# Kernel optimization log

Hardware: AMD Instinct MI355X
Metric: run time of the kernel (lower is better)

## Reference

```python
import jax, jax.numpy as jnp
import numpy as np
import math

V, S, E, H, L, B = 50257, 1024, 768, 12, 12, 4
D = E // H
EPS = 1e-5


def setup_inputs() -> dict:
    key = jax.random.key(0)
    ks = jax.random.split(key, 20)
    sd = 0.02
    inp = {
        "idx": jax.random.randint(ks[0], (B, S), 0, V),
        "targets": jax.random.randint(ks[1], (B, S), 0, V),
        "wte": jax.random.normal(ks[2], (V, E), jnp.float32) * sd,  # tied with lm_head
        "wpe": jax.random.normal(ks[3], (S, E), jnp.float32) * sd,
        "ln1_g": jnp.ones((L, E), jnp.float32),
        "ln1_b": jnp.zeros((L, E), jnp.float32),
        "attn_w": jax.random.normal(ks[4], (L, E, 3 * E), jnp.float32) * sd,
        "attn_b": jnp.zeros((L, 3 * E), jnp.float32),
        "proj_w": jax.random.normal(ks[5], (L, E, E), jnp.float32) * (sd / math.sqrt(2 * L)),
        "proj_b": jnp.zeros((L, E), jnp.float32),
        "ln2_g": jnp.ones((L, E), jnp.float32),
        "ln2_b": jnp.zeros((L, E), jnp.float32),
        "fc_w": jax.random.normal(ks[6], (L, E, 4 * E), jnp.float32) * sd,
        "fc_b": jnp.zeros((L, 4 * E), jnp.float32),
        "fcp_w": jax.random.normal(ks[7], (L, 4 * E, E), jnp.float32) * (sd / math.sqrt(2 * L)),
        "fcp_b": jnp.zeros((L, E), jnp.float32),
        "lnf_g": jnp.ones((E,), jnp.float32),
        "lnf_b": jnp.zeros((E,), jnp.float32),
    }
    return inp


def layer_norm(x, g, b):
    mu = jnp.mean(x, axis=-1, keepdims=True)
    var = jnp.mean(jnp.square(x - mu), axis=-1, keepdims=True)
    return (x - mu) * jax.lax.rsqrt(var + EPS) * g + b


def reference(idx, targets, wte, wpe, ln1_g, ln1_b, attn_w, attn_b, proj_w, proj_b,
              ln2_g, ln2_b, fc_w, fc_b, fcp_w, fcp_b, lnf_g, lnf_b):
    seq = idx.shape[1]
    x = wte[idx] + wpe[:seq]  # [B,S,E]
    mask = jnp.tril(jnp.ones((seq, seq), bool))
    scale = 1.0 / math.sqrt(D)

    def block(x, p):
        l1g, l1b, aw, ab, pw, pb, l2g, l2b, fw, fb, fpw, fpb = p
        h = layer_norm(x, l1g, l1b)
        qkv = h @ aw + ab  # [B,S,3E]
        q, k, v = jnp.split(qkv, 3, axis=-1)
        q = q.reshape(-1, seq, H, D).transpose(0, 2, 1, 3)  # [B,H,S,D]
        k = k.reshape(-1, seq, H, D).transpose(0, 2, 1, 3)
        v = v.reshape(-1, seq, H, D).transpose(0, 2, 1, 3)
        scores = jnp.einsum('bhqd,bhkd->bhqk', q, k) * scale
        scores = jnp.where(mask, scores, -jnp.inf)
        attn = jax.nn.softmax(scores, axis=-1)
        y = jnp.einsum('bhqk,bhkd->bhqd', attn, v)
        y = y.transpose(0, 2, 1, 3).reshape(-1, seq, E)
        x = x + y @ pw + pb
        h2 = layer_norm(x, l2g, l2b)
        h2 = jax.nn.gelu(h2 @ fw + fb, approximate=False)
        x = x + h2 @ fpw + fpb
        return x, None

    x, _ = jax.lax.scan(block, x, (ln1_g, ln1_b, attn_w, attn_b, proj_w, proj_b,
                                   ln2_g, ln2_b, fc_w, fc_b, fcp_w, fcp_b))
    x = layer_norm(x, lnf_g, lnf_b)
    logits = x @ wte.T  # tied lm_head, [B,S,V]
    logp = jax.nn.log_softmax(logits, axis=-1)
    loss = -jnp.mean(jnp.take_along_axis(logp, targets[..., None], axis=-1))
    return logits, loss
```

## Files before the change

### kernel.cpp

```cpp
#include <hip/hip_runtime.h>
#include <hip/hip_bf16.h>
#include <math.h>

#define V 50257
#define SQ 1024
#define E 768
#define NH 12
#define NL 12
#define NB 4
#define MR (NB*SQ)

typedef __bf16 bf16x8 __attribute__((ext_vector_type(8)));
typedef float f32x4 __attribute__((ext_vector_type(4)));
typedef unsigned short us8 __attribute__((ext_vector_type(8)));

__device__ __forceinline__ float b2f(unsigned short u) {
    union { float f; unsigned int i; } x; x.i = ((unsigned int)u) << 16; return x.f;
}
__device__ __forceinline__ unsigned short f2b(float f) {
    unsigned int u = __float_as_uint(f);
    u = (u + 0x7fff + ((u >> 16) & 1)) >> 16;
    return (unsigned short)u;
}
__device__ __forceinline__ void gload16(const unsigned short* g, unsigned short* l) {
    __builtin_amdgcn_global_load_lds((const __attribute__((address_space(1))) void*)g,
                                     (__attribute__((address_space(3))) void*)l, 16, 0, 0);
}

__global__ __launch_bounds__(256)
void embed_k(const int* __restrict__ idx, const float* __restrict__ wte,
             const float* __restrict__ wpe, float* __restrict__ x)
{
    int r = blockIdx.x, t = threadIdx.x;
    int tok = idx[r];
    int s = r & (SQ - 1);
    const float* wt = wte + (size_t)tok * E;
    const float* wp = wpe + (size_t)s * E;
    float* xr = x + (size_t)r * E;
    for (int e = t; e < E; e += 256) xr[e] = wt[e] + wp[e];
}

__global__ __launch_bounds__(256)
void ln_k(const float* __restrict__ x, const float* __restrict__ g,
          const float* __restrict__ bb, unsigned short* __restrict__ out)
{
    int r = blockIdx.x, t = threadIdx.x;
    int lane = t & 63, wid = t >> 6;
    const float* xr = x + (size_t)r * E;
    float v0 = xr[t], v1 = xr[t + 256], v2 = xr[t + 512];
    float s = v0 + v1 + v2;
    #pragma unroll
    for (int o = 1; o < 64; o <<= 1) s += __shfl_xor(s, o);
    __shared__ float red[8];
    if (lane == 0) red[wid] = s;
    __syncthreads();
    float mu = (red[0] + red[1] + red[2] + red[3]) * (1.f / E);
    float d0 = v0 - mu, d1 = v1 - mu, d2 = v2 - mu;
    float s2 = d0 * d0 + d1 * d1 + d2 * d2;
    #pragma unroll
    for (int o = 1; o < 64; o <<= 1) s2 += __shfl_xor(s2, o);
    if (lane == 0) red[wid + 4] = s2;
    __syncthreads();
    float rs = rsqrtf((red[4] + red[5] + red[6] + red[7]) * (1.f / E) + 1e-5f);
    unsigned short* orow = out + (size_t)r * E;
    orow[t]       = f2b(d0 * rs * g[t] + bb[t]);
    orow[t + 256] = f2b(d1 * rs * g[t + 256] + bb[t + 256]);
    orow[t + 512] = f2b(d2 * rs * g[t + 512] + bb[t + 512]);
}

__global__ __launch_bounds__(256)
void conv_k(const float* __restrict__ in, unsigned short* __restrict__ out, int n4)
{
    int i = blockIdx.x * 256 + threadIdx.x;
    int stride = gridDim.x * 256;
    for (; i < n4; i += stride) {
        float4 v = ((const float4*)in)[i];
        ushort4 o;
        o.x = f2b(v.x); o.y = f2b(v.y); o.z = f2b(v.z); o.w = f2b(v.w);
        ((ushort4*)out)[i] = o;
    }
}

__global__ __launch_bounds__(256)
void tconv_k(const float* __restrict__ in, unsigned short* __restrict__ out, int Kd, int Nd)
{
    __shared__ float tile[32][33];
    size_t loff = (size_t)blockIdx.z * Kd * Nd;
    in  += loff;
    out += loff;
    int n0 = blockIdx.x * 32, k0 = blockIdx.y * 32;
    int tc = threadIdx.x & 31, tr = threadIdx.x >> 5;
    #pragma unroll
    for (int i = 0; i < 4; ++i)
        tile[tr + i * 8][tc] = in[(size_t)(k0 + tr + i * 8) * Nd + n0 + tc];
    __syncthreads();
    #pragma unroll
    for (int i = 0; i < 4; ++i)
        out[(size_t)(n0 + tr + i * 8) * Kd + k0 + tc] = f2b(tile[tc][tr + i * 8]);
}

template<int EPI, bool DB, int MI, int NI, int MINW>
__global__ __launch_bounds__(256, MINW)
void gemm_k(const unsigned short* __restrict__ A, const unsigned short* __restrict__ B,
            const float* __restrict__ bias, const float* __restrict__ resid,
            void* __restrict__ Cv, unsigned short* __restrict__ vt,
            float2* __restrict__ part, int M, int N, int K, int Nreal)
{
    constexpr int NBUF = DB ? 2 : 1;
    constexpr int BM = 32 * MI, BN = 32 * NI;
    __shared__ __align__(16) unsigned short As[NBUF][BM * 64];
    __shared__ __align__(16) unsigned short Bs[NBUF][BN * 64];
    const int t = threadIdx.x;
    const int lane = t & 63, wv = t >> 6;
    const int wr = wv >> 1, wc = wv & 1;
    const int m0 = blockIdx.x * BM, n0 = blockIdx.y * BN;
    const int ntile = blockIdx.y;
    const int lq = lane & 15, lg = lane >> 4;

    f32x4 acc[MI][NI];
    const f32x4 fz = {0.f, 0.f, 0.f, 0.f};
    #pragma unroll
    for (int i = 0; i < MI; ++i)
        #pragma unroll
        for (int j = 0; j < NI; ++j) acc[i][j] = fz;

    const int srow = t >> 3, sc = t & 7;

    auto stage = [&](int buf, int k0) {
        #pragma unroll
        for (int i = 0; i < MI; ++i) {
            int row = srow + i * 32;
            int gc = ((sc ^ (row & 7)) << 3);
            gload16(A + (size_t)(m0 + row) * K + k0 + gc, &As[buf][row * 64 + sc * 8]);
        }
        #pragma unroll
        for (int i = 0; i < NI; ++i) {
            int row = srow + i * 32;
            int gc = ((sc ^ (row & 7)) << 3);
            int nrow = n0 + row;
            if (EPI == 3 && nrow >= Nreal) nrow = Nreal - 1;
            gload16(B + (size_t)nrow * K + k0 + gc, &Bs[buf][row * 64 + sc * 8]);
        }
    };
    auto compute = [&](int buf) {
        #pragma unroll
        for (int ks = 0; ks < 64; ks += 32) {
            bf16x8 af[MI], bfr[NI];
            #pragma unroll
            for (int mi = 0; mi < MI; ++mi) {
                int row = wr * (16 * MI) + mi * 16 + lq;
                int c = (ks >> 3) + lg;
                af[mi] = *(const bf16x8*)&As[buf][row * 64 + ((c ^ (row & 7)) << 3)];
            }
            #pragma unroll
            for (int ni = 0; ni < NI; ++ni) {
                int row = wc * (16 * NI) + ni * 16 + lq;
                int c = (ks >> 3) + lg;
                bfr[ni] = *(const bf16x8*)&Bs[buf][row * 64 + ((c ^ (row & 7)) << 3)];
            }
            #pragma unroll
            for (int mi = 0; mi < MI; ++mi)
                #pragma unroll
                for (int ni = 0; ni < NI; ++ni)
                    acc[mi][ni] = __builtin_amdgcn_mfma_f32_16x16x32_bf16(
                        af[mi], bfr[ni], acc[mi][ni], 0, 0, 0);
        }
    };

    const int KT = K >> 6;
    if constexpr (DB) {
        stage(0, 0);
        __syncthreads();
        int cur = 0;
        for (int kt = 0; kt < KT; ++kt) {
            if (kt + 1 < KT) stage(cur ^ 1, (kt + 1) << 6);
            compute(cur);
            __syncthreads();
            cur ^= 1;
        }
    } else {
        for (int kt = 0; kt < KT; ++kt) {
            stage(0, kt << 6);
            __syncthreads();
            compute(0);
            __syncthreads();
        }
    }

    const int colb = n0 + wc * (16 * NI) + lq;
    const int rowb = m0 + wr * (16 * MI) + lg * 4;

    if constexpr (EPI == 3) {
        __shared__ float2 Ls[2][BM / 2][2];
        float* C = (float*)Cv;
        #pragma unroll
        for (int mi = 0; mi < MI; ++mi) {
            #pragma unroll
            for (int j = 0; j < 4; ++j) {
                int row = rowb + mi * 16 + j;
                float v[NI];
                #pragma unroll
                for (int ni = 0; ni < NI; ++ni) {
                    int col = colb + ni * 16;
                    float vv = acc[mi][ni][j];
                    if (col < Nreal) C[(size_t)row * Nreal + col] = vv;
                    else vv = -1e30f;
                    v[ni] = vv;
                }
                float lm = v[0];
                #pragma unroll
                for (int ni = 1; ni < NI; ++ni) lm = fmaxf(lm, v[ni]);
                #pragma unroll
                for (int o = 1; o < 16; o <<= 1) lm = fmaxf(lm, __shfl_xor(lm, o));
                float ls = 0.f;
                #pragma unroll
                for (int ni = 0; ni < NI; ++ni) ls += __expf(v[ni] - lm);
                #pragma unroll
                for (int o = 1; o < 16; o <<= 1) ls += __shfl_xor(ls, o);
                if (lq == 0) Ls[wr][mi * 16 + lg * 4 + j][wc] = make_float2(lm, ls);
            }
        }
        __syncthreads();
        if (t < BM) {
            float2 a = Ls[t / (BM / 2)][t % (BM / 2)][0];
            float2 b = Ls[t / (BM / 2)][t % (BM / 2)][1];
            float mm = fmaxf(a.x, b.x);
            float ss = a.y * __expf(a.x - mm) + b.y * __expf(b.x - mm);
            part[(size_t)ntile * MR + m0 + t] = make_float2(mm, ss);
        }
    } else if constexpr (EPI == 0) {
        unsigned short* C = (unsigned short*)Cv;
        #pragma unroll
        for (int mi = 0; mi < MI; ++mi) {
            int r0 = rowb + mi * 16;
            #pragma unroll
            for (int ni = 0; ni < NI; ++ni) {
                int col = colb + ni * 16;
                float b4 = bias[col];
                float vals[4];
                #pragma unroll
                for (int j = 0; j < 4; ++j) vals[j] = acc[mi][ni][j] + b4;
                #pragma unroll
                for (int j = 0; j < 4; ++j)
                    C[(size_t)(r0 + j) * N + col] = f2b(vals[j]);
                if (col >= 2 * E) {
                    int d = col - 2 * E; int hh = d >> 6; d &= 63;
                    int bb2 = r0 >> 10, kv = r0 & (SQ - 1);
                    unsigned int lo = (unsigned int)f2b(vals[0]) | ((unsigned int)f2b(vals[1]) << 16);
                    unsigned int hi = (unsigned int)f2b(vals[2]) | ((unsigned int)f2b(vals[3]) << 16);
                    uint2 u; u.x = lo; u.y = hi;
                    *(uint2*)&vt[(((size_t)bb2 * NH + hh) * 64 + d) * SQ + kv] = u;
                }
            }
        }
    } else {
        #pragma unroll
        for (int mi = 0; mi < MI; ++mi) {
            #pragma unroll
            for (int ni = 0; ni < NI; ++ni) {
                int col = colb + ni * 16;
                #pragma unroll
                for (int j = 0; j < 4; ++j) {
                    int row = rowb + mi * 16 + j;
                    float v = acc[mi][ni][j] + bias[col];
                    if constexpr (EPI == 1) {
                        ((float*)Cv)[(size_t)row * N + col] =
                            v + resid[(size_t)row * N + col];
                    } else {
                        float u = v + 0.044715f * v * v * v;
                        float e = __expf(-1.5957691216f * u);
                        v = v / (1.f + e);
                        ((unsigned short*)Cv)[(size_t)row * N + col] = f2b(v);
                    }
                }
            }
        }
    }
}

__global__ __launch_bounds__(256)
void attn_k(const unsigned short* __restrict__ qkv, const unsigned short* __restrict__ vtg,
            unsigned short* __restrict__ y)
{
    const int bid = blockIdx.x;
    const int qb  = (SQ / 64 - 1) - (bid / 48);
    const int bh  = bid % 48;
    const int h = bh % NH, b = bh / NH;
    const int t = threadIdx.x, lane = t & 63, wid = t >> 6;
    const int q0 = qb * 64;
    const int lq = lane & 15, lg = lane >> 4;

    __shared__ __align__(16) unsigned short Ks[2][64 * 72];
    __shared__ __align__(16) unsigned short Vs[2][64 * 72];
    __shared__ __align__(16) unsigned short Ps[4][16 * 72];

    const unsigned short* base  = qkv + (size_t)b * SQ * 2304;
    const unsigned short* vbase = vtg + (size_t)bh * 64 * SQ;

    const int qrow = q0 + wid * 16 + lq;
    bf16x8 qf0 = *(const bf16x8*)(base + (size_t)qrow * 2304 + h * 64 + lg * 8);
    bf16x8 qf1 = *(const bf16x8*)(base + (size_t)qrow * 2304 + h * 64 + 32 + lg * 8);

    const int sr = t >> 3, sc = t & 7;
    us8 ka, kb, va, vb;
    {
        const unsigned short* kp = base + (size_t)sr * 2304 + 768 + h * 64 + sc * 8;
        ka = *(const us8*)kp;
        kb = *(const us8*)(kp + (size_t)32 * 2304);
        const unsigned short* vp = vbase + (size_t)sr * SQ + sc * 8;
        va = *(const us8*)vp;
        vb = *(const us8*)(vp + (size_t)32 * SQ);
    }
    *(us8*)&Ks[0][sr * 72 + sc * 8] = ka;
    *(us8*)&Ks[0][(sr + 32) * 72 + sc * 8] = kb;
    *(us8*)&Vs[0][sr * 72 + sc * 8] = va;
    *(us8*)&Vs[0][(sr + 32) * 72 + sc * 8] = vb;
    __syncthreads();

    f32x4 of[4];
    const f32x4 fz = {0.f, 0.f, 0.f, 0.f};
    #pragma unroll
    for (int i = 0; i < 4; ++i) of[i] = fz;
    float mreg = -1e30f, lreg = 0.f;

    int cur = 0;
    for (int tt = 0; tt <= qb; ++tt) {
        if (tt < qb) {
            int kv0n = (tt + 1) * 64;
            const unsigned short* kp = base + (size_t)(kv0n + sr) * 2304 + 768 + h * 64 + sc * 8;
            ka = *(const us8*)kp;
            kb = *(const us8*)(kp + (size_t)32 * 2304);
            const unsigned short* vp = vbase + (size_t)sr * SQ + kv0n + sc * 8;
            va = *(const us8*)vp;
            vb = *(const us8*)(vp + (size_t)32 * SQ);
        }
        const unsigned short* Ksc = Ks[cur];
        const unsigned short* Vsc = Vs[cur];

        f32x4 sf[4];
        #pragma unroll
        for (int mi = 0; mi < 4; ++mi) sf[mi] = fz;
        #pragma unroll
        for (int mi = 0; mi < 4; ++mi) {
            const unsigned short* kr = &Ksc[(mi * 16 + lq) * 72 + lg * 8];
            bf16x8 k0 = *(const bf16x8*)kr;
            bf16x8 k1 = *(const bf16x8*)(kr + 32);
            sf[mi] = __builtin_amdgcn_mfma_f32_16x16x32_bf16(k0, qf0, sf[mi], 0, 0, 0);
            sf[mi] = __builtin_amdgcn_mfma_f32_16x16x32_bf16(k1, qf1, sf[mi], 0, 0, 0);
        }

        float pv[16];
        const int kvb = tt * 64 + lg * 4;
        #pragma unroll
        for (int mi = 0; mi < 4; ++mi)
            #pragma unroll
            for (int j = 0; j < 4; ++j) {
                float s = sf[mi][j] * 0.125f;
                if (tt == qb && (kvb + mi * 16 + j) > qrow) s = -1e30f;
                pv[mi * 4 + j] = s;
            }
        float tm = pv[0];
        #pragma unroll
        for (int i = 1; i < 16; ++i) tm = fmaxf(tm, pv[i]);
        tm = fmaxf(tm, __shfl_xor(tm, 16));
        tm = fmaxf(tm, __shfl_xor(tm, 32));
        float mn  = fmaxf(mreg, tm);
        float fac = __expf(mreg - mn);
        float ts = 0.f;
        #pragma unroll
        for (int i = 0; i < 16; ++i) { float p = __expf(pv[i] - mn); pv[i] = p; ts += p; }
        ts += __shfl_xor(ts, 16);
        ts += __shfl_xor(ts, 32);
        lreg = lreg * fac + ts;
        mreg = mn;
        #pragma unroll
        for (int j = 0; j < 4; ++j) {
            float fj = __shfl(fac, 20 * lg + j);
            of[0][j] *= fj; of[1][j] *= fj; of[2][j] *= fj; of[3][j] *= fj;
        }
        unsigned short* pw = &Ps[wid][lq * 72];
        #pragma unroll
        for (int mi = 0; mi < 4; ++mi) {
            unsigned int lo = (unsigned int)f2b(pv[mi * 4 + 0]) | ((unsigned int)f2b(pv[mi * 4 + 1]) << 16);
            unsigned int hi = (unsigned int)f2b(pv[mi * 4 + 2]) | ((unsigned int)f2b(pv[mi * 4 + 3]) << 16);
            uint2 u; u.x = lo; u.y = hi;
            *(uint2*)&pw[mi * 16 + lg * 4] = u;
        }
        #pragma unroll
        for (int ks = 0; ks < 2; ++ks) {
            bf16x8 pf = *(const bf16x8*)&Ps[wid][lq * 72 + ks * 32 + lg * 8];
            #pragma unroll
            for (int ni = 0; ni < 4; ++ni) {
                bf16x8 vf = *(const bf16x8*)&Vsc[(ni * 16 + lq) * 72 + ks * 32 + lg * 8];
                of[ni] = __builtin_amdgcn_mfma_f32_16x16x32_bf16(pf, vf, of[ni], 0, 0, 0);
            }
        }
        if (tt < qb) {
            int nb = cur ^ 1;
            *(us8*)&Ks[nb][sr * 72 + sc * 8] = ka;
            *(us8*)&Ks[nb][(sr + 32) * 72 + sc * 8] = kb;
            *(us8*)&Vs[nb][sr * 72 + sc * 8] = va;
            *(us8*)&Vs[nb][(sr + 32) * 72 + sc * 8] = vb;
        }
        __syncthreads();
        cur ^= 1;
    }

    float inv = 1.f / lreg;
    #pragma unroll
    for (int j = 0; j < 4; ++j) {
        float fj = __shfl(inv, 20 * lg + j);
        int row = q0 + wid * 16 + lg * 4 + j;
        unsigned short* yr = y + ((size_t)b * SQ + row) * E + h * 64 + lq;
        #pragma unroll
        for (int ni = 0; ni < 4; ++ni)
            yr[ni * 16] = f2b(of[ni][j] * fj);
    }
}

__global__ __launch_bounds__(256)
void lossred_k(const float2* __restrict__ part, const float* __restrict__ logits,
               const int* __restrict__ tgt, float* __restrict__ rl, int NT)
{
    int t = threadIdx.x, lane = t & 63, wid = t >> 6;
    int r = blockIdx.x * 4 + wid;
    float m = -1e30f, s = 0.f;
    for (int nt = lane; nt < NT; nt += 64) {
        float2 p = part[(size_t)nt * MR + r];
        float mm = fmaxf(m, p.x);
        s = s * __expf(m - mm) + p.y * __expf(p.x - mm);
        m = mm;
    }
    #pragma unroll
    for (int o = 1; o < 64; o <<= 1) {
        float m2 = __shfl_xor(m, o), s2 = __shfl_xor(s, o);
        float mm = fmaxf(m, m2);
        s = s * __expf(m - mm) + s2 * __expf(m2 - mm);
        m = mm;
    }
    if (lane == 0)
        rl[r] = __logf(s) + m - logits[(size_t)r * V + tgt[r]];
}

__global__ __launch_bounds__(256)
void finloss_k(const float* __restrict__ rl, float* __restrict__ out)
{
    __shared__ float red[256];
    int t = threadIdx.x;
    float s = 0.f;
    for (int i = t; i < MR; i += 256) s += rl[i];
    red[t] = s; __syncthreads();
    for (int o = 128; o > 0; o >>= 1) { if (t < o) red[t] += red[t + o]; __syncthreads(); }
    if (t == 0) out[0] = red[0] * (1.f / MR);
}

extern "C" void kernel_launch(void* const* d_in, const int* in_sizes, int n_in,
                              void* d_out, int out_size, void* d_ws, size_t ws_size,
                              hipStream_t stream)
{
    const int*   idx    = (const int*)  d_in[0];
    const int*   tgt    = (const int*)  d_in[1];
    const float* wte    = (const float*)d_in[2];
    const float* wpe    = (const float*)d_in[3];
    const float* ln1_g  = (const float*)d_in[4];
    const float* ln1_b  = (const float*)d_in[5];
    const float* attn_w = (const float*)d_in[6];
    const float* attn_b = (const float*)d_in[7];
    const float* proj_w = (const float*)d_in[8];
    const float* proj_b = (const float*)d_in[9];
    const float* ln2_g  = (const float*)d_in[10];
    const float* ln2_b  = (const float*)d_in[11];
    const float* fc_w   = (const float*)d_in[12];
    const float* fc_b   = (const float*)d_in[13];
    const float* fcp_w  = (const float*)d_in[14];
    const float* fcp_b  = (const float*)d_in[15];
    const float* lnf_g  = (const float*)d_in[16];
    const float* lnf_b  = (const float*)d_in[17];

    unsigned char* p = (unsigned char*)d_ws;
    auto alloc = [&](size_t bytes) {
        unsigned char* r = p; p += (bytes + 255) & ~(size_t)255; return r;
    };
    float*          x    = (float*)         alloc((size_t)MR * E * 4);
    unsigned short* h    = (unsigned short*)alloc((size_t)MR * E * 2);
    unsigned short* qkv  = (unsigned short*)alloc((size_t)MR * 3 * E * 2);
    unsigned short* yb   = (unsigned short*)alloc((size_t)MR * E * 2);
    unsigned short* act  = (unsigned short*)alloc((size_t)MR * 4 * E * 2);
    unsigned short* wteb = (unsigned short*)alloc((size_t)V * E * 2);
    unsigned short* vtg  = (unsigned short*)alloc((size_t)NB * NH * 64 * SQ * 2);
    float2*         part = (float2*)        alloc((size_t)197 * MR * 8);
    float*          rl   = (float*)         alloc((size_t)MR * 4);

    size_t used = (size_t)(p - (unsigned char*)d_ws);
    size_t perL = (size_t)12 * E * E * 2 + 4 * 256;
    int NLW = (ws_size >= used + (size_t)NL * perL) ? NL : 1;
    unsigned short* wqA  = (unsigned short*)alloc((size_t)NLW * 3 * E * E * 2);
    unsigned short* wpA  = (unsigned short*)alloc((size_t)NLW * E * E * 2);
    unsigned short* wfA  = (unsigned short*)alloc((size_t)NLW * 4 * E * E * 2);
    unsigned short* wfpA = (unsigned short*)alloc((size_t)NLW * 4 * E * E * 2);

    float* logits = (float*)d_out;
    float* lossp  = logits + (size_t)MR * V;

    embed_k<<<MR, 256, 0, stream>>>(idx, wte, wpe, x);
    conv_k<<<2048, 256, 0, stream>>>(wte, wteb, (int)((size_t)V * E / 4));

    if (NLW == NL) {
        tconv_k<<<dim3(3 * E / 32, E / 32, NL), 256, 0, stream>>>(attn_w, wqA, E, 3 * E);
        tconv_k<<<dim3(E / 32, E / 32, NL), 256, 0, stream>>>(proj_w, wpA, E, E);
        tconv_k<<<dim3(4 * E / 32, E / 32, NL), 256, 0, stream>>>(fc_w, wfA, E, 4 * E);
        tconv_k<<<dim3(E / 32, 4 * E / 32, NL), 256, 0, stream>>>(fcp_w, wfpA, 4 * E, E);
    }

    for (int l = 0; l < NL; ++l) {
        int lw = (NLW == NL) ? l : 0;
        unsigned short* wq  = wqA  + (size_t)lw * 3 * E * E;
        unsigned short* wp  = wpA  + (size_t)lw * E * E;
        unsigned short* wf  = wfA  + (size_t)lw * 4 * E * E;
        unsigned short* wfp = wfpA + (size_t)lw * 4 * E * E;
        if (NLW != NL) {
            tconv_k<<<dim3(3 * E / 32, E / 32), 256, 0, stream>>>(
                attn_w + (size_t)l * E * 3 * E, wq, E, 3 * E);
            tconv_k<<<dim3(E / 32, E / 32), 256, 0, stream>>>(
                proj_w + (size_t)l * E * E, wp, E, E);
            tconv_k<<<dim3(4 * E / 32, E / 32), 256, 0, stream>>>(
                fc_w + (size_t)l * E * 4 * E, wf, E, 4 * E);
            tconv_k<<<dim3(E / 32, 4 * E / 32), 256, 0, stream>>>(
                fcp_w + (size_t)l * 4 * E * E, wfp, 4 * E, E);
        }

        ln_k<<<MR, 256, 0, stream>>>(x, ln1_g + l * E, ln1_b + l * E, h);
        gemm_k<0, false, 4, 4, 3><<<dim3(32, 18), 256, 0, stream>>>(
            h, wq, attn_b + (size_t)l * 3 * E, nullptr, qkv, vtg, nullptr,
            MR, 3 * E, E, 3 * E);
        attn_k<<<768, 256, 0, stream>>>(qkv, vtg, yb);
        gemm_k<1, false, 2, 4, 3><<<dim3(64, 6), 256, 0, stream>>>(
            yb, wp, proj_b + (size_t)l * E, x, x, nullptr, nullptr, MR, E, E, E);
        ln_k<<<MR, 256, 0, stream>>>(x, ln2_g + l * E, ln2_b + l * E, h);
        gemm_k<2, false, 4, 4, 3><<<dim3(32, 24), 256, 0, stream>>>(
            h, wf, fc_b + (size_t)l * 4 * E, nullptr, act, nullptr, nullptr,
            MR, 4 * E, E, 4 * E);
        gemm_k<1, false, 2, 4, 3><<<dim3(64, 6), 256, 0, stream>>>(
            act, wfp, fcp_b + (size_t)l * E, x, x, nullptr, nullptr, MR, E, 4 * E, E);
    }

    ln_k<<<MR, 256, 0, stream>>>(x, lnf_g, lnf_b, h);
    gemm_k<3, false, 2, 8, 3><<<dim3(64, 197), 256, 0, stream>>>(
        h, wteb, nullptr, nullptr, logits, nullptr, part, MR, 50304, E, V);

    lossred_k<<<MR / 4, 256, 0, stream>>>(part, logits, tgt, rl, 197);
    finloss_k<<<1, 256, 0, stream>>>(rl, lossp);
}
```

Before: 2.676 ms.

## Add dedicated LM-head GEMM kernel with triple-buffered async loads and larger tiles

```diff
diff --git a/kernel.cpp b/kernel.cpp
--- a/kernel.cpp
+++ b/kernel.cpp
@@ -26,6 +26,8 @@
     __builtin_amdgcn_global_load_lds((const __attribute__((address_space(1))) void*)g,
                                      (__attribute__((address_space(3))) void*)l, 16, 0, 0);
 }
+
+#define VMWAIT(n) asm volatile("s_waitcnt vmcnt(" #n ")" ::: "memory")
 
 __global__ __launch_bounds__(256)
 void embed_k(const int* __restrict__ idx, const float* __restrict__ wte,
@@ -104,7 +106,7 @@
 void gemm_k(const unsigned short* __restrict__ A, const unsigned short* __restrict__ B,
             const float* __restrict__ bias, const float* __restrict__ resid,
             void* __restrict__ Cv, unsigned short* __restrict__ vt,
-            float2* __restrict__ part, int M, int N, int K, int Nreal)
+            int M, int N, int K)
 {
     constexpr int NBUF = DB ? 2 : 1;
     constexpr int BM = 32 * MI, BN = 32 * NI;
@@ -114,7 +116,6 @@
     const int lane = t & 63, wv = t >> 6;
     const int wr = wv >> 1, wc = wv & 1;
     const int m0 = blockIdx.x * BM, n0 = blockIdx.y * BN;
-    const int ntile = blockIdx.y;
     const int lq = lane & 15, lg = lane >> 4;
 
     f32x4 acc[MI][NI];
@@ -137,9 +138,7 @@
         for (int i = 0; i < NI; ++i) {
             int row = srow + i * 32;
             int gc = ((sc ^ (row & 7)) << 3);
-            int nrow = n0 + row;
-            if (EPI == 3 && nrow >= Nreal) nrow = Nreal - 1;
-            gload16(B + (size_t)nrow * K + k0 + gc, &Bs[buf][row * 64 + sc * 8]);
+            gload16(B + (size_t)(n0 + row) * K + k0 + gc, &Bs[buf][row * 64 + sc * 8]);
         }
     };
     auto compute = [&](int buf) {
@@ -190,45 +189,7 @@
     const int colb = n0 + wc * (16 * NI) + lq;
     const int rowb = m0 + wr * (16 * MI) + lg * 4;
 
-    if constexpr (EPI == 3) {
-        __shared__ float2 Ls[2][BM / 2][2];
-        float* C = (float*)Cv;
-        #pragma unroll
-        for (int mi = 0; mi < MI; ++mi) {
-            #pragma unroll
-            for (int j = 0; j < 4; ++j) {
-                int row = rowb + mi * 16 + j;
-                float v[NI];
-                #pragma unroll
-                for (int ni = 0; ni < NI; ++ni) {
-                    int col = colb + ni * 16;
-                    float vv = acc[mi][ni][j];
-                    if (col < Nreal) C[(size_t)row * Nreal + col] = vv;
-                    else vv = -1e30f;
-                    v[ni] = vv;
-                }
-                float lm = v[0];
-                #pragma unroll
-                for (int ni = 1; ni < NI; ++ni) lm = fmaxf(lm, v[ni]);
-                #pragma unroll
-                for (int o = 1; o < 16; o <<= 1) lm = fmaxf(lm, __shfl_xor(lm, o));
-                float ls = 0.f;
-                #pragma unroll
-                for (int ni = 0; ni < NI; ++ni) ls += __expf(v[ni] - lm);
-                #pragma unroll
-                for (int o = 1; o < 16; o <<= 1) ls += __shfl_xor(ls, o);
-                if (lq == 0) Ls[wr][mi * 16 + lg * 4 + j][wc] = make_float2(lm, ls);
-            }
-        }
-        __syncthreads();
-        if (t < BM) {
-            float2 a = Ls[t / (BM / 2)][t % (BM / 2)][0];
-            float2 b = Ls[t / (BM / 2)][t % (BM / 2)][1];
-            float mm = fmaxf(a.x, b.x);
-            float ss = a.y * __expf(a.x - mm) + b.y * __expf(b.x - mm);
-            part[(size_t)ntile * MR + m0 + t] = make_float2(mm, ss);
-        }
-    } else if constexpr (EPI == 0) {
+    if constexpr (EPI == 0) {
         unsigned short* C = (unsigned short*)Cv;
         #pragma unroll
         for (int mi = 0; mi < MI; ++mi) {
@@ -275,6 +236,125 @@
                 }
             }
         }
+    }
+}
+
+__global__ __launch_bounds__(512, 2)
+void lmhead_k(const unsigned short* __restrict__ A, const unsigned short* __restrict__ B,
+              float* __restrict__ C, float2* __restrict__ part, int Nreal)
+{
+    constexpr int K = 768, KT = 12;
+    __shared__ __align__(16) unsigned short As[3][128 * 64];
+    __shared__ __align__(16) unsigned short Bs[3][256 * 64];
+    __shared__ float2 Ls[2][64][4];
+
+    const int t = threadIdx.x;
+    const int lane = t & 63, wv = t >> 6;
+    const int wr = wv >> 2, wc = wv & 3;
+    const int m0 = blockIdx.x * 128, n0 = blockIdx.y * 256;
+    const int lq = lane & 15, lg = lane >> 4;
+    const int srow = t >> 3, sc = t & 7;
+
+    f32x4 acc[4][4];
+    const f32x4 fz = {0.f, 0.f, 0.f, 0.f};
+    #pragma unroll
+    for (int i = 0; i < 4; ++i)
+        #pragma unroll
+        for (int j = 0; j < 4; ++j) acc[i][j] = fz;
+
+    auto stage = [&](int slot, int k0) {
+        #pragma unroll
+        for (int i = 0; i < 2; ++i) {
+            int row = srow + i * 64;
+            int gc = ((sc ^ (row & 7)) << 3);
+            gload16(A + (size_t)(m0 + row) * K + k0 + gc, &As[slot][row * 64 + sc * 8]);
+        }
+        #pragma unroll
+        for (int i = 0; i < 4; ++i) {
+            int row = srow + i * 64;
+            int gc = ((sc ^ (row & 7)) << 3);
+            int nrow = n0 + row;
+            if (nrow >= Nreal) nrow = Nreal - 1;
+            gload16(B + (size_t)nrow * K + k0 + gc, &Bs[slot][row * 64 + sc * 8]);
+        }
+    };
+    auto compute = [&](int slot) {
+        #pragma unroll
+        for (int ks = 0; ks < 64; ks += 32) {
+            bf16x8 af[4], bfr[4];
+            #pragma unroll
+            for (int mi = 0; mi < 4; ++mi) {
+                int row = wr * 64 + mi * 16 + lq;
+                int c = (ks >> 3) + lg;
+                af[mi] = *(const bf16x8*)&As[slot][row * 64 + ((c ^ (row & 7)) << 3)];
+            }
+            #pragma unroll
+            for (int ni = 0; ni < 4; ++ni) {
+                int row = wc * 64 + ni * 16 + lq;
+                int c = (ks >> 3) + lg;
+                bfr[ni] = *(const bf16x8*)&Bs[slot][row * 64 + ((c ^ (row & 7)) << 3)];
+            }
+            #pragma unroll
+            for (int mi = 0; mi < 4; ++mi)
+                #pragma unroll
+                for (int ni = 0; ni < 4; ++ni)
+                    acc[mi][ni] = __builtin_amdgcn_mfma_f32_16x16x32_bf16(
+                        af[mi], bfr[ni], acc[mi][ni], 0, 0, 0);
+        }
+    };
+
+    stage(0, 0); stage(1, 64); stage(2, 128);
+
+    for (int kt = 0; kt < KT; ++kt) {
+        if (kt < KT - 2)      VMWAIT(12);
+        else if (kt == KT - 2) VMWAIT(6);
+        else                   VMWAIT(0);
+        __builtin_amdgcn_sched_barrier(0);
+        __builtin_amdgcn_s_barrier();
+        __builtin_amdgcn_sched_barrier(0);
+        compute(kt % 3);
+        __builtin_amdgcn_sched_barrier(0);
+        __builtin_amdgcn_s_barrier();
+        __builtin_amdgcn_sched_barrier(0);
+        if (kt + 3 < KT) stage(kt % 3, (kt + 3) << 6);
+    }
+
+    const int colb = n0 + wc * 64 + lq;
+    const int rowb = m0 + wr * 64 + lg * 4;
+    #pragma unroll
+    for (int mi = 0; mi < 4; ++mi) {
+        #pragma unroll
+        for (int j = 0; j < 4; ++j) {
+            int row = rowb + mi * 16 + j;
+            float v[4];
+            #pragma unroll
+            for (int ni = 0; ni < 4; ++ni) {
+                int col = colb + ni * 16;
+                float vv = acc[mi][ni][j];
+                if (col < Nreal) C[(size_t)row * Nreal + col] = vv;
+                else vv = -1e30f;
+                v[ni] = vv;
+            }
+            float lm = fmaxf(fmaxf(v[0], v[1]), fmaxf(v[2], v[3]));
+            #pragma unroll
+            for (int o = 1; o < 16; o <<= 1) lm = fmaxf(lm, __shfl_xor(lm, o));
+            float ls = __expf(v[0] - lm) + __expf(v[1] - lm)
+                     + __expf(v[2] - lm) + __expf(v[3] - lm);
+            #pragma unroll
+            for (int o = 1; o < 16; o <<= 1) ls += __shfl_xor(ls, o);
+            if (lq == 0) Ls[wr][mi * 16 + lg * 4 + j][wc] = make_float2(lm, ls);
+        }
+    }
+    __syncthreads();
+    if (t < 128) {
+        float2 a = Ls[t >> 6][t & 63][0];
+        float2 b = Ls[t >> 6][t & 63][1];
+        float2 c = Ls[t >> 6][t & 63][2];
+        float2 d = Ls[t >> 6][t & 63][3];
+        float mm = fmaxf(fmaxf(a.x, b.x), fmaxf(c.x, d.x));
+        float ss = a.y * __expf(a.x - mm) + b.y * __expf(b.x - mm)
+                 + c.y * __expf(c.x - mm) + d.y * __expf(d.x - mm);
+        part[(size_t)blockIdx.y * MR + m0 + t] = make_float2(mm, ss);
     }
 }
 
@@ -531,22 +611,19 @@
 
         ln_k<<<MR, 256, 0, stream>>>(x, ln1_g + l * E, ln1_b + l * E, h);
         gemm_k<0, false, 4, 4, 3><<<dim3(32, 18), 256, 0, stream>>>(
-            h, wq, attn_b + (size_t)l * 3 * E, nullptr, qkv, vtg, nullptr,
-            MR, 3 * E, E, 3 * E);
+            h, wq, attn_b + (size_t)l * 3 * E, nullptr, qkv, vtg, MR, 3 * E, E);
         attn_k<<<768, 256, 0, stream>>>(qkv, vtg, yb);
         gemm_k<1, false, 2, 4, 3><<<dim3(64, 6), 256, 0, stream>>>(
-            yb, wp, proj_b + (size_t)l * E, x, x, nullptr, nullptr, MR, E, E, E);
+            yb, wp, proj_b + (size_t)l * E, x, x, nullptr, MR, E, E);
         ln_k<<<MR, 256, 0, stream>>>(x, ln2_g + l * E, ln2_b + l * E, h);
         gemm_k<2, false, 4, 4, 3><<<dim3(32, 24), 256, 0, stream>>>(
-            h, wf, fc_b + (size_t)l * 4 * E, nullptr, act, nullptr, nullptr,
-            MR, 4 * E, E, 4 * E);
+            h, wf, fc_b + (size_t)l * 4 * E, nullptr, act, nullptr, MR, 4 * E, E);
         gemm_k<1, false, 2, 4, 3><<<dim3(64, 6), 256, 0, stream>>>(
-            act, wfp, fcp_b + (size_t)l * E, x, x, nullptr, nullptr, MR, E, 4 * E, E);
+            act, wfp, fcp_b + (size_t)l * E, x, x, nullptr, MR, E, 4 * E);
     }
 
     ln_k<<<MR, 256, 0, stream>>>(x, lnf_g, lnf_b, h);
-    gemm_k<3, false, 2, 8, 3><<<dim3(64, 197), 256, 0, stream>>>(
-        h, wteb, nullptr, nullptr, logits, nullptr, part, MR, 50304, E, V);
+    lmhead_k<<<dim3(32, 197), 512, 0, stream>>>(h, wteb, logits, part, V);
 
     lossred_k<<<MR / 4, 256, 0, stream>>>(part, logits, tgt, rl, 197);
     finloss_k<<<1, 256, 0, stream>>>(rl, lossp);
```

Measured after the change: 2.857 ms. +6.8%, slower.
